# Performance work log

Measured on AMD Instinct MI355X. Metric: run time of the kernel, lower is better.

## Reference

```python
import jax, jax.numpy as jnp
import numpy as np

B, T, V, H, DIN = 2048, 120, 9, 32, 1  # batch, HISTORY_BARS, BAR_DESCR, N_SKILLS, d_in


def setup_inputs() -> dict:
    key = jax.random.key(0)
    ks = jax.random.split(key, 5)
    s = 1.0 / np.sqrt(H)  # torch default init scale for LSTMCell / Linear
    return {
        "x": jax.random.normal(ks[0], (B, V * T), dtype=jnp.float32),
        "W_ih": jax.random.uniform(ks[1], (4 * H, DIN), jnp.float32, -s, s),
        "W_hh": jax.random.uniform(ks[2], (4 * H, H), jnp.float32, -s, s),
        "b_ih": jnp.zeros((4 * H,), jnp.float32),
        "b_hh": jnp.zeros((4 * H,), jnp.float32),
        "W_cg_x": jax.random.uniform(ks[3], (H, DIN), jnp.float32, -s, s),
        "W_cg_h": jax.random.uniform(ks[4], (H, H), jnp.float32, -s, s),
        "b_cg": jnp.zeros((H,), jnp.float32),
    }


def reference(x, W_ih, W_hh, b_ih, b_hh, W_cg_x, W_cg_h, b_cg):
    batch = x.shape[0]
    # [batch, V*T] -> [batch*V, T, 1]; each of the 9 variables is an
    # independent length-120 sequence run through the same CGLSTM cell.
    xs = x.reshape(batch * V, T, DIN)
    # Precompute the input-dependent projections for all timesteps at once.
    x_gates = jnp.einsum('btd,gd->btg', xs, W_ih) + b_ih  # [BV, T, 4H]
    x_cg = jnp.einsum('btd,hd->bth', xs, W_cg_x)          # [BV, T, H]

    def step(carry, inp):
        h, c = carry
        xg, xc = inp
        gates = xg + h @ W_hh.T + b_hh
        i, f, g, o = jnp.split(gates, 4, axis=-1)  # torch LSTMCell gate order
        i = jax.nn.sigmoid(i)
        f = jax.nn.sigmoid(f)
        g = jnp.tanh(g)
        o = jax.nn.sigmoid(o)
        c_new = f * c + i * g
        # contextual gate uses the PREVIOUS hidden state h
        cg = jax.nn.sigmoid(xc + h @ W_cg_h.T + b_cg)
        h_new = cg * jnp.tanh(c_new)  # gated output replaces h in the state
        return (h_new, c_new), None

    init = (jnp.zeros((batch * V, H), x.dtype), jnp.zeros((batch * V, H), x.dtype))
    (h_final, _), _ = jax.lax.scan(
        step, init, (x_gates.transpose(1, 0, 2), x_cg.transpose(1, 0, 2)))
    # torch.cat over variables -> var-major layout [batch, V*H]
    return h_final.reshape(batch, V * H)
```

## Files before the change

kernel.cpp:

```cpp
#include <hip/hip_runtime.h>


constexpr int T = 120;
constexpr int H = 32;
constexpr int NSEQ = 2048 * 9;
constexpr int SEQ_PER_BLOCK = 16;
constexpr int BLOCK = 64;

typedef _Float16 f16;
typedef _Float16 f16x8 __attribute__((ext_vector_type(8)));
typedef float f32x4 __attribute__((ext_vector_type(4)));

#define LOG2E 1.4426950408889634f

__device__ __forceinline__ float fast_rcp(float x) {
    return __builtin_amdgcn_rcpf(x);
}
__device__ __forceinline__ float fast_exp2(float x) {
    return __builtin_amdgcn_exp2f(x);
}
__device__ __forceinline__ float sigmoid_f(float x) {
    return fast_rcp(1.0f + fast_exp2(-LOG2E * x));
}
__device__ __forceinline__ float tanh_f(float x) {
    return fmaf(-2.0f, fast_rcp(1.0f + fast_exp2(2.0f * LOG2E * x)), 1.0f);
}

__global__ __launch_bounds__(BLOCK, 1)
void cglstm_mfma_kernel(
    const float* __restrict__ x,
    const float* __restrict__ W_ih,
    const float* __restrict__ W_hh,
    const float* __restrict__ b_ih,
    const float* __restrict__ b_hh,
    const float* __restrict__ W_cg_x,
    const float* __restrict__ W_cg_h,
    const float* __restrict__ b_cg,
    float* __restrict__ out)
{
    __shared__ float xsT[T * 16];
    __shared__ __align__(16) f16 hbuf[64 * 8];

    const int l   = threadIdx.x;
    const int m15 = l & 15;
    const int g   = l >> 4;
    const int sb  = blockIdx.x * SEQ_PER_BLOCK;

    {
        const float* xb = x + (size_t)sb * T;
        for (int i = l; i < SEQ_PER_BLOCK * T; i += BLOCK) {
            int s = i / T;
            int t = i - s * T;
            xsT[t * 16 + s] = xb[i];
        }
    }

    f16x8 bt[8];
    #pragma unroll
    for (int tile = 0; tile < 8; ++tile) {
        const float* wrow = (tile < 6)
            ? (W_hh   + (size_t)(tile * 16 + m15) * H + 8 * g)
            : (W_cg_h + (size_t)((tile - 6) * 16 + m15) * H + 8 * g);
        f32x4 wa = *(const f32x4*)(wrow);
        f32x4 wb = *(const f32x4*)(wrow + 4);
        bt[tile] = f16x8{(f16)wa.x, (f16)wa.y, (f16)wa.z, (f16)wa.w,
                         (f16)wb.x, (f16)wb.y, (f16)wb.z, (f16)wb.w};
    }

    float w_in[8], bias[8];
    #pragma unroll
    for (int tile = 0; tile < 8; ++tile) {
        const int n = tile * 16 + m15;
        if (tile < 6) { w_in[tile] = W_ih[n];        bias[tile] = b_ih[n] + b_hh[n]; }
        else          { w_in[tile] = W_cg_x[n - 96]; bias[tile] = b_cg[n - 96]; }
    }

    const int slot_r = (l & ~3) | ((l ^ (l >> 3)) & 3);
    int waddr[2][4];
    #pragma unroll
    for (int p = 0; p < 2; ++p) {
        #pragma unroll
        for (int r = 0; r < 4; ++r) {
            const int lp = ((2 * p + (m15 >> 3)) << 4) | (4 * g + r);
            const int sp = (lp & ~3) | ((lp ^ (lp >> 3)) & 3);
            waddr[p][r] = sp * 16 + (m15 & 7) * 2;
        }
    }

    *(f16x8*)(hbuf + slot_r * 8) = f16x8{0, 0, 0, 0, 0, 0, 0, 0};
    __syncthreads();

    float c_st[2][4] = {};
    char* hbase = (char*)hbuf;

    #pragma unroll 1
    for (int t = 0; t < T; ++t) {
        const f32x4 xq = *(const f32x4*)(xsT + t * 16 + 4 * g);
        const f16x8 af = *(const f16x8*)(hbuf + slot_r * 8);

        f32x4 d[8];
        #pragma unroll
        for (int tile = 0; tile < 8; ++tile) {
            f32x4 cin;
            cin.x = fmaf(xq.x, w_in[tile], bias[tile]);
            cin.y = fmaf(xq.y, w_in[tile], bias[tile]);
            cin.z = fmaf(xq.z, w_in[tile], bias[tile]);
            cin.w = fmaf(xq.w, w_in[tile], bias[tile]);
            d[tile] = __builtin_amdgcn_mfma_f32_16x16x32_f16(af, bt[tile], cin, 0, 0, 0);
        }

        #pragma unroll
        for (int p = 0; p < 2; ++p) {
            #pragma unroll
            for (int r = 0; r < 4; ++r) {
                const float ig = sigmoid_f(d[0 + p][r]);
                const float fg = sigmoid_f(d[2 + p][r]);
                const float gg = tanh_f(d[4 + p][r]);
                const float cg = sigmoid_f(d[6 + p][r]);
                const float cv = fmaf(fg, c_st[p][r], ig * gg);
                c_st[p][r] = cv;
                const f16 hf = (f16)(cg * tanh_f(cv));
                *(f16*)(hbase + waddr[p][r]) = hf;
            }
        }
    }

    const f16x8 hfin = *(const f16x8*)(hbuf + slot_r * 8);
    float* orow = out + (size_t)(sb + m15) * H + 8 * g;
    #pragma unroll
    for (int j = 0; j < 8; ++j) orow[j] = (float)hfin[j];
}

extern "C" void kernel_launch(void* const* d_in, const int* in_sizes, int n_in,
                              void* d_out, int out_size, void* d_ws, size_t ws_size,
                              hipStream_t stream) {
    const float* x      = (const float*)d_in[0];
    const float* W_ih   = (const float*)d_in[1];
    const float* W_hh   = (const float*)d_in[2];
    const float* b_ih   = (const float*)d_in[3];
    const float* b_hh   = (const float*)d_in[4];
    const float* W_cg_x = (const float*)d_in[5];
    const float* W_cg_h = (const float*)d_in[6];
    const float* b_cg   = (const float*)d_in[7];
    float* out = (float*)d_out;

    const int grid = NSEQ / SEQ_PER_BLOCK;
    cglstm_mfma_kernel<<<grid, BLOCK, 0, stream>>>(
        x, W_ih, W_hh, b_ih, b_hh, W_cg_x, W_cg_h, b_cg, out);
}
```

Measured before the change: 237.3 us.

## Split hidden units across two waves with double-buffered h and barriers

Each block now runs two wavefronts. Each wave handles 16 of the 32 hidden units, so each wave issues 4 MFMAs per step instead of 8 and does half the gate math. The hidden state sits in a double-buffered LDS array and a __syncthreads runs every timestep so both waves see the full h. The final output is written from fp32 registers rather than the f16 buffer. This shortens the serial per-step critical path at the cost of a block barrier per step and twice the threads per block.

```diff
diff --git a/kernel.cpp b/kernel.cpp
--- a/kernel.cpp
+++ b/kernel.cpp
@@ -5,7 +5,7 @@
 constexpr int H = 32;
 constexpr int NSEQ = 2048 * 9;
 constexpr int SEQ_PER_BLOCK = 16;
-constexpr int BLOCK = 64;
+constexpr int BLOCK = 128;
 
 typedef _Float16 f16;
 typedef _Float16 f16x8 __attribute__((ext_vector_type(8)));
@@ -26,8 +26,12 @@
     return fmaf(-2.0f, fast_rcp(1.0f + fast_exp2(2.0f * LOG2E * x)), 1.0f);
 }
 
+__device__ __forceinline__ int slot_swz(int L) {
+    return (L & ~3) | ((L ^ (L >> 3)) & 3);
+}
+
 __global__ __launch_bounds__(BLOCK, 1)
-void cglstm_mfma_kernel(
+void cglstm_kernel(
     const float* __restrict__ x,
     const float* __restrict__ W_ih,
     const float* __restrict__ W_hh,
@@ -39,96 +43,98 @@
     float* __restrict__ out)
 {
     __shared__ float xsT[T * 16];
-    __shared__ __align__(16) f16 hbuf[64 * 8];
+    __shared__ __align__(16) f16 hbuf[2][64 * 8];
 
-    const int l   = threadIdx.x;
+    const int tid = threadIdx.x;
+    const int wv  = tid >> 6;
+    const int l   = tid & 63;
     const int m15 = l & 15;
     const int g   = l >> 4;
     const int sb  = blockIdx.x * SEQ_PER_BLOCK;
 
     {
         const float* xb = x + (size_t)sb * T;
-        for (int i = l; i < SEQ_PER_BLOCK * T; i += BLOCK) {
+        for (int i = tid; i < SEQ_PER_BLOCK * T; i += BLOCK) {
             int s = i / T;
             int t = i - s * T;
             xsT[t * 16 + s] = xb[i];
         }
     }
+    if (tid < 64) ((uint4*)&hbuf[0][0])[tid] = uint4{0, 0, 0, 0};
 
-    f16x8 bt[8];
+    const int ncol = wv * 16 + m15;
+    f16x8 bt[4];
+    float w_in[4], bias[4];
     #pragma unroll
-    for (int tile = 0; tile < 8; ++tile) {
-        const float* wrow = (tile < 6)
-            ? (W_hh   + (size_t)(tile * 16 + m15) * H + 8 * g)
-            : (W_cg_h + (size_t)((tile - 6) * 16 + m15) * H + 8 * g);
-        f32x4 wa = *(const f32x4*)(wrow);
+    for (int gate = 0; gate < 4; ++gate) {
+        const float* wrow = (gate < 3)
+            ? (W_hh   + (size_t)(gate * 32 + ncol) * H + 8 * g)
+            : (W_cg_h + (size_t)ncol * H + 8 * g);
+        f32x4 wa = *(const f32x4*)wrow;
         f32x4 wb = *(const f32x4*)(wrow + 4);
-        bt[tile] = f16x8{(f16)wa.x, (f16)wa.y, (f16)wa.z, (f16)wa.w,
+        bt[gate] = f16x8{(f16)wa.x, (f16)wa.y, (f16)wa.z, (f16)wa.w,
                          (f16)wb.x, (f16)wb.y, (f16)wb.z, (f16)wb.w};
-    }
-
-    float w_in[8], bias[8];
-    #pragma unroll
-    for (int tile = 0; tile < 8; ++tile) {
-        const int n = tile * 16 + m15;
-        if (tile < 6) { w_in[tile] = W_ih[n];        bias[tile] = b_ih[n] + b_hh[n]; }
-        else          { w_in[tile] = W_cg_x[n - 96]; bias[tile] = b_cg[n - 96]; }
-    }
-
-    const int slot_r = (l & ~3) | ((l ^ (l >> 3)) & 3);
-    int waddr[2][4];
-    #pragma unroll
-    for (int p = 0; p < 2; ++p) {
-        #pragma unroll
-        for (int r = 0; r < 4; ++r) {
-            const int lp = ((2 * p + (m15 >> 3)) << 4) | (4 * g + r);
-            const int sp = (lp & ~3) | ((lp ^ (lp >> 3)) & 3);
-            waddr[p][r] = sp * 16 + (m15 & 7) * 2;
+        if (gate < 3) {
+            w_in[gate] = W_ih[gate * 32 + ncol];
+            bias[gate] = b_ih[gate * 32 + ncol] + b_hh[gate * 32 + ncol];
+        } else {
+            w_in[gate] = W_cg_x[ncol];
+            bias[gate] = b_cg[ncol];
         }
     }
 
-    *(f16x8*)(hbuf + slot_r * 8) = f16x8{0, 0, 0, 0, 0, 0, 0, 0};
+    const int rdoff = slot_swz(g * 16 + m15) * 16;
+    int wroff[4];
+    #pragma unroll
+    for (int r = 0; r < 4; ++r) {
+        const int kq = 2 * wv + (m15 >> 3);
+        const int Lw = kq * 16 + 4 * g + r;
+        wroff[r] = slot_swz(Lw) * 16 + (m15 & 7) * 2;
+    }
+
     __syncthreads();
 
-    float c_st[2][4] = {};
-    char* hbase = (char*)hbuf;
+    float c_st[4] = {0.0f, 0.0f, 0.0f, 0.0f};
+    float h_keep[4] = {0.0f, 0.0f, 0.0f, 0.0f};
+    int cur = 0;
 
     #pragma unroll 1
     for (int t = 0; t < T; ++t) {
         const f32x4 xq = *(const f32x4*)(xsT + t * 16 + 4 * g);
-        const f16x8 af = *(const f16x8*)(hbuf + slot_r * 8);
+        const f16x8 af = *(const f16x8*)((const char*)&hbuf[cur][0] + rdoff);
 
-        f32x4 d[8];
+        f32x4 d[4];
         #pragma unroll
-        for (int tile = 0; tile < 8; ++tile) {
-            f32x4 cin;
-            cin.x = fmaf(xq.x, w_in[tile], bias[tile]);
-            cin.y = fmaf(xq.y, w_in[tile], bias[tile]);
-            cin.z = fmaf(xq.z, w_in[tile], bias[tile]);
-            cin.w = fmaf(xq.w, w_in[tile], bias[tile]);
-            d[tile] = __builtin_amdgcn_mfma_f32_16x16x32_f16(af, bt[tile], cin, 0, 0, 0);
+        for (int gate = 0; gate < 4; ++gate) {
+            f32x4 acc;
+            acc.x = fmaf(xq.x, w_in[gate], bias[gate]);
+            acc.y = fmaf(xq.y, w_in[gate], bias[gate]);
+            acc.z = fmaf(xq.z, w_in[gate], bias[gate]);
+            acc.w = fmaf(xq.w, w_in[gate], bias[gate]);
+            d[gate] = __builtin_amdgcn_mfma_f32_16x16x32_f16(af, bt[gate], acc, 0, 0, 0);
         }
 
+        char* wbase = (char*)&hbuf[cur ^ 1][0];
         #pragma unroll
-        for (int p = 0; p < 2; ++p) {
-            #pragma unroll
-            for (int r = 0; r < 4; ++r) {
-                const float ig = sigmoid_f(d[0 + p][r]);
-                const float fg = sigmoid_f(d[2 + p][r]);
-                const float gg = tanh_f(d[4 + p][r]);
-                const float cg = sigmoid_f(d[6 + p][r]);
-                const float cv = fmaf(fg, c_st[p][r], ig * gg);
-                c_st[p][r] = cv;
-                const f16 hf = (f16)(cg * tanh_f(cv));
-                *(f16*)(hbase + waddr[p][r]) = hf;
-            }
+        for (int r = 0; r < 4; ++r) {
+            const float ig = sigmoid_f(d[0][r]);
+            const float fg = sigmoid_f(d[1][r]);
+            const float gg = tanh_f(d[2][r]);
+            const float cg = sigmoid_f(d[3][r]);
+            const float cv = fmaf(fg, c_st[r], ig * gg);
+            c_st[r] = cv;
+            const float hv = cg * tanh_f(cv);
+            h_keep[r] = hv;
+            *(f16*)(wbase + wroff[r]) = (f16)hv;
         }
+
+        __syncthreads();
+        cur ^= 1;
     }
 
-    const f16x8 hfin = *(const f16x8*)(hbuf + slot_r * 8);
-    float* orow = out + (size_t)(sb + m15) * H + 8 * g;
     #pragma unroll
-    for (int j = 0; j < 8; ++j) orow[j] = (float)hfin[j];
+    for (int r = 0; r < 4; ++r)
+        out[(size_t)(sb + 4 * g + r) * H + ncol] = h_keep[r];
 }
 
 extern "C" void kernel_launch(void* const* d_in, const int* in_sizes, int n_in,
@@ -145,6 +151,6 @@
     float* out = (float*)d_out;
 
     const int grid = NSEQ / SEQ_PER_BLOCK;
-    cglstm_mfma_kernel<<<grid, BLOCK, 0, stream>>>(
+    cglstm_kernel<<<grid, BLOCK, 0, stream>>>(
         x, W_ih, W_hh, b_ih, b_hh, W_cg_x, W_cg_h, b_cg, out);
 }
```

Result: faster. 207.8 us (-12.4%).
